# Optimization experiments

Measured on AMD Instinct MI355X. Metric: run time of the kernel, lower is better.

The kernel has to match this reference:

```python
import jax, jax.numpy as jnp
import numpy as np

D, L, C, CP, H, HD, QB, KB = 8, 2048, 128, 16, 4, 32, 32, 128
NQ = L // QB

def _ln(x, eps=1e-5):
    m = jnp.mean(x, axis=-1, keepdims=True)
    v = jnp.var(x, axis=-1, keepdims=True)
    return (x - m) * jax.lax.rsqrt(v + eps)

def _ada_ln(a, s, Wg, bg, Ws):
    # AF3 AdaLN: gated layernorm conditioned on s
    an = _ln(a); sn = _ln(s)
    return jax.nn.sigmoid(sn @ Wg + bg) * an + sn @ Ws

def setup_inputs() -> dict:
    key = jax.random.key(0)
    ks = jax.random.split(key, 32)
    p = lambda i, shape: jax.random.normal(ks[i], shape, dtype=jnp.float32) * 0.02
    inp = {}
    inp['A_I'] = jax.random.normal(ks[0], (D, L, C), dtype=jnp.float32)
    inp['S_I'] = jax.random.normal(ks[1], (D, L, C), dtype=jnp.float32)
    inp['Z_II'] = jax.random.normal(ks[2], (1, L, L, CP), dtype=jnp.float32)
    # static sliding-window indices: 128-key window centered on each 32-query block
    inp['indicesQ'] = jnp.arange(L, dtype=jnp.int64).reshape(NQ, QB)
    kraw = (jnp.arange(NQ) * QB - (KB - QB) // 2)[:, None] + jnp.arange(KB)[None, :]
    inp['indicesK'] = jnp.clip(kraw, 0, L - 1).astype(jnp.int64)
    inp['maskQ_float'] = jnp.zeros((NQ, QB), jnp.float32)
    inp['maskK_float'] = ((kraw < 0) | (kraw >= L)).astype(jnp.float32)
    # parameters
    inp['ada1_Wg'] = p(3, (C, C)); inp['ada1_bg'] = jnp.zeros((C,), jnp.float32); inp['ada1_Ws'] = p(4, (C, C))
    inp['Wq'] = p(5, (C, H * HD)); inp['bq'] = jnp.zeros((H * HD,), jnp.float32)
    inp['Wk'] = p(6, (C, H * HD)); inp['Wv'] = p(7, (C, H * HD))
    inp['ln0_g'] = jnp.ones((CP,), jnp.float32); inp['ln0_b'] = jnp.zeros((CP,), jnp.float32)
    inp['Wb'] = p(8, (CP, H))
    inp['Wg_attn'] = p(9, (C, H * HD))
    inp['Wa'] = p(10, (H * HD, C))
    inp['Wop'] = p(11, (C, C)); inp['bop'] = jnp.full((C,), -2.0, jnp.float32)
    inp['ada2_Wg'] = p(12, (C, C)); inp['ada2_bg'] = jnp.zeros((C,), jnp.float32); inp['ada2_Ws'] = p(13, (C, C))
    inp['W_sw'] = p(14, (C, 2 * C)); inp['W_lin'] = p(15, (C, 2 * C))
    inp['ct_Wg'] = p(16, (C, C)); inp['ct_bg'] = jnp.full((C,), -2.0, jnp.float32)
    inp['W_out2'] = p(17, (2 * C, C))
    return inp

def _forward(A_I, S_I, Z_II, indicesQ, indicesK, maskQ_float, maskK_float,
             ada1_Wg, ada1_bg, ada1_Ws, Wq, bq, Wk, Wv, ln0_g, ln0_b, Wb,
             Wg_attn, Wa, Wop, bop, ada2_Wg, ada2_bg, ada2_Ws, W_sw, W_lin,
             ct_Wg, ct_bg, W_out2):
    Dn, Lv = A_I.shape[0], A_I.shape[1]
    An = _ada_ln(A_I, S_I, ada1_Wg, ada1_bg, ada1_Ws)
    Q = (An @ Wq + bq).reshape(Dn, Lv, H, HD)
    K = (An @ Wk).reshape(Dn, Lv, H, HD)
    V = (An @ Wv).reshape(Dn, Lv, H, HD)
    B = ((_ln(Z_II) * ln0_g + ln0_b) @ Wb)[0]        # [L, L, H]
    G = jax.nn.sigmoid(An @ Wg_attn).reshape(Dn, Lv, H, HD)
    qs = Q[:, indicesQ]                              # [D, nq, qb, H, hd]
    ksub = K[:, indicesK]                            # [D, nq, kb, H, hd]
    vs = V[:, indicesK]
    attn = jnp.einsum('dnihc,dnjhc->dnijh', qs, ksub) / jnp.sqrt(jnp.float32(HD))
    bias = B[indicesQ[:, :, None], indicesK[:, None, :]]  # [nq, qb, kb, H]
    attn = attn + bias[None]
    mask = maskQ_float[None, :, :, None, None] + maskK_float[None, :, None, :, None]
    attn = attn - 1e9 * mask
    attn = jax.nn.softmax(attn, axis=-2)             # softmax over key window (j)
    af = jnp.einsum('dnijh,dnjhc->dnihc', attn, vs)
    af = af * (1.0 - maskQ_float)[None, :, :, None, None]
    af = af.reshape(Dn, -1, H, HD)[:, :Lv]
    af = (G * af).reshape(Dn, Lv, H * HD) @ Wa
    B_I = jax.nn.sigmoid(S_I @ Wop + bop) * af
    A = A_I + B_I
    an2 = _ada_ln(A, S_I, ada2_Wg, ada2_bg, ada2_Ws)
    b = jax.nn.silu(an2 @ W_sw) * (an2 @ W_lin)      # SwiGLU transition
    A = A + jax.nn.sigmoid(S_I @ ct_Wg + ct_bg) * (b @ W_out2)
    return A

def reference(A_I, S_I, Z_II, indicesQ, indicesK, maskQ_float, maskK_float,
              ada1_Wg, ada1_bg, ada1_Ws, Wq, bq, Wk, Wv, ln0_g, ln0_b, Wb,
              Wg_attn, Wa, Wop, bop, ada2_Wg, ada2_bg, ada2_Ws, W_sw, W_lin,
              ct_Wg, ct_bg, W_out2):
    return _forward(A_I, S_I, Z_II, indicesQ, indicesK, maskQ_float, maskK_float,
                    ada1_Wg, ada1_bg, ada1_Ws, Wq, bq, Wk, Wv, ln0_g, ln0_b, Wb,
                    Wg_attn, Wa, Wop, bop, ada2_Wg, ada2_bg, ada2_Ws, W_sw, W_lin,
                    ct_Wg, ct_bg, W_out2)
```

## Files before the change

kernel.cpp:

```cpp
#include <hip/hip_runtime.h>

#define DL 16384
#define LL 2048
#define NQB 64
#define QBS 32
#define KBS 128

typedef __attribute__((ext_vector_type(8))) short short8;
typedef __attribute__((ext_vector_type(4))) short short4v;
typedef __attribute__((ext_vector_type(4))) float f32x4;

__device__ __forceinline__ float sigmoidf_(float x) { return 1.f / (1.f + expf(-x)); }

__device__ __forceinline__ short f2bf(float f) {
    union { float f; unsigned u; } v; v.f = f;
    unsigned r = (v.u + 0x7FFFu + ((v.u >> 16) & 1u)) >> 16;
    return (short)r;
}
__device__ __forceinline__ unsigned f2bfu(float f) {
    union { float f; unsigned u; } v; v.f = f;
    return (v.u + 0x7FFFu + ((v.u >> 16) & 1u)) >> 16;
}
__device__ __forceinline__ float bf2f(short h) {
    union { unsigned u; float f; } v; v.u = ((unsigned)(unsigned short)h) << 16;
    return v.f;
}
__device__ __forceinline__ unsigned packbf16(short a, short b) {
    return ((unsigned)(unsigned short)a) | (((unsigned)(unsigned short)b) << 16);
}

#define AFRAG(buf, stride, r0, kk) (*(const short8*)&(buf)[(size_t)((r0) + cl) * (stride) + (kk) * 32 + kg * 8])
#define WFRAG(Wt, K, n0, kk) (*(const short8*)((Wt) + (size_t)((n0) + cl) * (K) + (kk) * 32 + kg * 8))
#define MFMA(acc, a, b) acc = __builtin_amdgcn_mfma_f32_16x16x32_bf16(a, b, acc, 0, 0, 0)

__global__ __launch_bounds__(256) void k_prep(
    const float* __restrict__ W0, const float* __restrict__ W1, const float* __restrict__ W2,
    const float* __restrict__ W3, const float* __restrict__ W4, const float* __restrict__ W5,
    const float* __restrict__ W6, const float* __restrict__ W7, const float* __restrict__ W8,
    const float* __restrict__ W9, const float* __restrict__ W10,
    const float* __restrict__ Wsw, const float* __restrict__ Wlin, const float* __restrict__ Wout2,
    const float* __restrict__ Z, const float* __restrict__ g16, const float* __restrict__ b16,
    const float* __restrict__ Wb,
    short* __restrict__ wout, short* __restrict__ BBt)
{
    __shared__ float sW[128 * 128];
    __shared__ float sWb[64], sg[16], sb[16];
    __shared__ short sT[4 * 4 * 128];
    const int b = blockIdx.x;
    const int tid = threadIdx.x;

    if (b < 17) {
        const float* srcs[14] = {W0,W1,W2,W3,W4,W5,W6,W7,W8,W9,W10,Wsw,Wlin,Wout2};
        const int sel[17]  = {0,1,2,3,4,5,6,7,8,9,10,11,11,12,12,13,13};
        const int soff[17] = {0,0,0,0,0,0,0,0,0,0,0, 0,128, 0,128, 0,16384};
        const int sN[17]   = {128,128,128,128,128,128,128,128,128,128,128, 256,256,256,256, 128,128};
        const int doff[17] = {0,16384,32768,49152,65536,81920,98304,114688,131072,147456,163840,
                              180224,196608, 212992,229376, 245760,245888};
        const int dK[17]   = {128,128,128,128,128,128,128,128,128,128,128, 128,128,128,128, 256,256};
        const float* src = srcs[sel[b]] + soff[b];
        const int srcN = sN[b];
        short* dst = wout + doff[b];
        const int dstK = dK[b];
        {
            const int r = tid >> 1, ch = (tid & 1) * 64;
            #pragma unroll
            for (int u = 0; u < 16; ++u) {
                float4 v = *(const float4*)(src + (size_t)r * srcN + ch + u * 4);
                *(float4*)&sW[r * 128 + ch + u * 4] = v;
            }
        }
        __syncthreads();
        {
            const int o = tid >> 1, kh = (tid & 1) * 64;
            #pragma unroll
            for (int u8 = 0; u8 < 8; ++u8) {
                short8 pk;
                #pragma unroll
                for (int e = 0; e < 8; ++e)
                    pk[e] = f2bf(sW[(kh + u8 * 8 + e) * 128 + o]);
                *(short8*)(dst + (size_t)o * dstK + kh + u8 * 8) = pk;
            }
        }
    } else {
        const int bb = b - 17;
        const int n = bb >> 3;
        const int io = (bb & 7) * 4;
        if (tid < 64) sWb[tid] = Wb[tid];
        if (tid < 16) { sg[tid] = g16[tid]; sb[tid] = b16[tid]; }
        __syncthreads();
        #pragma unroll
        for (int p = 0; p < 2; ++p) {
            int pair = tid + 256 * p;
            int il = pair >> 7, j = pair & 127;
            int i = io + il;
            int kr = n * 32 - 48 + j;
            int kc = min(max(kr, 0), LL - 1);
            const float4* z4 = (const float4*)(Z + ((long)(n * 32 + i) * LL + kc) * 16);
            float zv[16];
            #pragma unroll
            for (int w = 0; w < 4; ++w) {
                float4 v = z4[w];
                zv[w * 4 + 0] = v.x; zv[w * 4 + 1] = v.y; zv[w * 4 + 2] = v.z; zv[w * 4 + 3] = v.w;
            }
            float sm = 0.f, sq = 0.f;
            #pragma unroll
            for (int cp = 0; cp < 16; ++cp) { sm += zv[cp]; sq = fmaf(zv[cp], zv[cp], sq); }
            float m = sm * (1.f / 16.f);
            float rs = rsqrtf(sq * (1.f / 16.f) - m * m + 1e-5f);
            float b0 = 0.f, b1 = 0.f, b2 = 0.f, b3 = 0.f;
            #pragma unroll
            for (int cp = 0; cp < 16; ++cp) {
                float zn = (zv[cp] - m) * rs * sg[cp] + sb[cp];
                b0 = fmaf(zn, sWb[cp * 4 + 0], b0);
                b1 = fmaf(zn, sWb[cp * 4 + 1], b1);
                b2 = fmaf(zn, sWb[cp * 4 + 2], b2);
                b3 = fmaf(zn, sWb[cp * 4 + 3], b3);
            }
            sT[(0 * 4 + il) * 128 + j] = f2bf(b0);
            sT[(1 * 4 + il) * 128 + j] = f2bf(b1);
            sT[(2 * 4 + il) * 128 + j] = f2bf(b2);
            sT[(3 * 4 + il) * 128 + j] = f2bf(b3);
        }
        __syncthreads();
        #pragma unroll
        for (int rr = 0; rr < 2; ++rr) {
            int cid = tid + rr * 256;
            int hh = cid >> 7, j = cid & 127;
            short4v pk;
            #pragma unroll
            for (int e = 0; e < 4; ++e) pk[e] = sT[(hh * 4 + e) * 128 + j];
            *(short4v*)(BBt + (((size_t)n * 4 + hh) * 128 + j) * 32 + io) = pk;
        }
    }
}

__global__ __launch_bounds__(512) void k_adaln_qkvg(
    const float* __restrict__ A_I, const float* __restrict__ S_I,
    const short* __restrict__ Wg1t, const short* __restrict__ Ws1t,
    const short* __restrict__ Wqt, const short* __restrict__ Wkt,
    const short* __restrict__ Wvt, const short* __restrict__ Wgat,
    const float* __restrict__ bg1, const float* __restrict__ bq,
    short* __restrict__ Qo, short* __restrict__ Ko, short* __restrict__ Vo, short* __restrict__ Go)
{
    __shared__ short sAr[32 * 136];
    __shared__ short sSn[32 * 136];
    __shared__ short sAn[32 * 136];
    __shared__ float sMean[32], sRstd[32];
    const int tid = threadIdx.x;
    const int lane = tid & 63;
    const long t0 = (long)blockIdx.x * 32;

    {
        const int row = tid >> 4, seg = tid & 15;
        const float* ap = A_I + (t0 + row) * 128 + seg * 8;
        const float* sp = S_I + (t0 + row) * 128 + seg * 8;
        float av[8], sv[8];
        #pragma unroll
        for (int u = 0; u < 2; ++u) {
            float4 a4 = ((const float4*)ap)[u];
            float4 s4 = ((const float4*)sp)[u];
            av[4*u] = a4.x; av[4*u+1] = a4.y; av[4*u+2] = a4.z; av[4*u+3] = a4.w;
            sv[4*u] = s4.x; sv[4*u+1] = s4.y; sv[4*u+2] = s4.z; sv[4*u+3] = s4.w;
        }
        float am = 0.f, aq = 0.f, sm = 0.f, sq = 0.f;
        #pragma unroll
        for (int u = 0; u < 8; ++u) {
            am += av[u]; aq = fmaf(av[u], av[u], aq);
            sm += sv[u]; sq = fmaf(sv[u], sv[u], sq);
        }
        am += __shfl_xor(am, 1); am += __shfl_xor(am, 2); am += __shfl_xor(am, 4); am += __shfl_xor(am, 8);
        aq += __shfl_xor(aq, 1); aq += __shfl_xor(aq, 2); aq += __shfl_xor(aq, 4); aq += __shfl_xor(aq, 8);
        sm += __shfl_xor(sm, 1); sm += __shfl_xor(sm, 2); sm += __shfl_xor(sm, 4); sm += __shfl_xor(sm, 8);
        sq += __shfl_xor(sq, 1); sq += __shfl_xor(sq, 2); sq += __shfl_xor(sq, 4); sq += __shfl_xor(sq, 8);
        float amean = am * (1.f / 128.f);
        float arstd = rsqrtf(aq * (1.f / 128.f) - amean * amean + 1e-5f);
        float smean = sm * (1.f / 128.f);
        float srstd = rsqrtf(sq * (1.f / 128.f) - smean * smean + 1e-5f);
        if ((tid & 15) == 0) { sMean[row] = amean; sRstd[row] = arstd; }
        short8 pa, ps;
        #pragma unroll
        for (int e = 0; e < 8; ++e) {
            pa[e] = f2bf(av[e]);
            ps[e] = f2bf((sv[e] - smean) * srstd);
        }
        *(short8*)&sAr[row * 136 + seg * 8] = pa;
        *(short8*)&sSn[row * 136 + seg * 8] = ps;
    }
    __syncthreads();
    const int w = tid >> 6;
    const int n0 = w * 16;
    const int cl = lane & 15, kg = lane >> 4;
    {
        short8 wg[4], wsf[4];
        #pragma unroll
        for (int kk = 0; kk < 4; ++kk) {
            wg[kk]  = WFRAG(Wg1t, 128, n0, kk);
            wsf[kk] = WFRAG(Ws1t, 128, n0, kk);
        }
        #pragma unroll
        for (int mt = 0; mt < 2; ++mt) {
            f32x4 ag = {0.f, 0.f, 0.f, 0.f}, as = {0.f, 0.f, 0.f, 0.f};
            #pragma unroll
            for (int kk = 0; kk < 4; ++kk) {
                short8 a = AFRAG(sSn, 136, mt * 16, kk);
                MFMA(ag, a, wg[kk]);
                MFMA(as, a, wsf[kk]);
            }
            const int col = n0 + cl;
            float bgc = bg1[col];
            #pragma unroll
            for (int i = 0; i < 4; ++i) {
                int r = mt * 16 + kg * 4 + i;
                float an = (bf2f(sAr[r * 136 + col]) - sMean[r]) * sRstd[r];
                float An = sigmoidf_(ag[i] + bgc) * an + as[i];
                sAn[r * 136 + col] = f2bf(An);
            }
        }
    }
    __syncthreads();
    {
        const float SCL = 0.17677669529663687f;
        short8 af[2][4];
        #pragma unroll
        for (int mt = 0; mt < 2; ++mt)
            #pragma unroll
            for (int kk = 0; kk < 4; ++kk)
                af[mt][kk] = AFRAG(sAn, 136, mt * 16, kk);
        #pragma unroll
        for (int m = 0; m < 4; ++m) {
            const short* Wt = (m == 0) ? Wqt : (m == 1) ? Wkt : (m == 2) ? Wvt : Wgat;
            short8 wf[4];
            #pragma unroll
            for (int kk = 0; kk < 4; ++kk) wf[kk] = WFRAG(Wt, 128, n0, kk);
            #pragma unroll
            for (int mt = 0; mt < 2; ++mt) {
                f32x4 acc = {0.f, 0.f, 0.f, 0.f};
                #pragma unroll
                for (int kk = 0; kk < 4; ++kk) MFMA(acc, af[mt][kk], wf[kk]);
                const int col = n0 + cl;
                #pragma unroll
                for (int i = 0; i < 4; ++i) {
                    long t = t0 + mt * 16 + kg * 4 + i;
                    float v = acc[i];
                    if (m == 0)      Qo[t * 128 + col] = f2bf((v + bq[col]) * SCL);
                    else if (m == 1) Ko[t * 128 + col] = f2bf(v);
                    else if (m == 2) Vo[t * 128 + col] = f2bf(v);
                    else             Go[t * 128 + col] = f2bf(sigmoidf_(v));
                }
            }
        }
    }
}

__global__ __launch_bounds__(512) void k_attn_postf(
    const short* __restrict__ Qg, const short* __restrict__ Kg, const short* __restrict__ Vg,
    const short* __restrict__ Gg, const short* __restrict__ BBt, const float* __restrict__ maskK,
    const float* __restrict__ S_I, const float* __restrict__ A_I,
    const short* __restrict__ Wat, const short* __restrict__ Wopt, const short* __restrict__ ctWgt,
    const short* __restrict__ Wg2t, const short* __restrict__ Ws2t,
    const short* __restrict__ Wswt, const short* __restrict__ Wlint, const short* __restrict__ Wout2t,
    const float* __restrict__ bop, const float* __restrict__ ctbg, const float* __restrict__ bg2,
    float* __restrict__ Out)
{
    __shared__ __align__(16) char smem[78336];
    short* sAF  = (short*)smem;
    short* vts  = (short*)(smem + 8704);
    short* Pl   = (short*)(smem + 43520);
    short* sS   = (short*)(smem + 8704);
    short* sSn  = (short*)(smem + 17408);
    float* sA   = (float*)(smem + 26112);
    float* sMean = (float*)(smem + 43008);
    float* sRstd = (float*)(smem + 43136);
    short* sAn2 = sAF;
    short* sB   = (short*)(smem + 8704);

    const int n = blockIdx.x, d = blockIdx.y;
    const int tid = threadIdx.x;
    const int lane = tid & 63;
    const long tb = (long)d * LL;
    const long t0 = tb + n * 32;
    const int kbase = n * 32 - 48;
    const int cl = lane & 15, kg = lane >> 4;
    const int w = tid >> 6;
    const int h = w >> 1, amt = w & 1;

    {
        const int unit = tid >> 1, half = tid & 1;
        const int hh = unit >> 6, j0 = (unit & 63) * 2;
        int kc0 = min(max(kbase + j0, 0), LL - 1);
        int kc1 = min(max(kbase + j0 + 1, 0), LL - 1);
        const short8* p0 = (const short8*)(Vg + (tb + kc0) * 128 + hh * 32 + half * 16);
        const short8* p1 = (const short8*)(Vg + (tb + kc1) * 128 + hh * 32 + half * 16);
        short8 e0 = p0[0], e1 = p0[1];
        short8 o0 = p1[0], o1 = p1[1];
        short* vh = vts + hh * 4352;
        #pragma unroll
        for (int e = 0; e < 8; ++e)
            *(unsigned*)&vh[(half * 16 + e) * 136 + j0] = packbf16(e0[e], o0[e]);
        #pragma unroll
        for (int e = 0; e < 8; ++e)
            *(unsigned*)&vh[(half * 16 + 8 + e) * 136 + j0] = packbf16(e1[e], o1[e]);
    }

    float sc[8][4];
    {
        short8 qf = *(const short8*)(Qg + (t0 + amt * 16 + cl) * 128 + h * 32 + kg * 8);
        #pragma unroll
        for (int nt = 0; nt < 8; ++nt) {
            const int key = nt * 16 + cl;
            int kc = min(max(kbase + key, 0), LL - 1);
            short8 kf = *(const short8*)(Kg + (tb + kc) * 128 + h * 32 + kg * 8);
            float mk = maskK[n * 128 + key] * 1e9f;
            f32x4 s = {0.f, 0.f, 0.f, 0.f};
            MFMA(s, qf, kf);
            short4v bfr = *(const short4v*)(BBt + (((size_t)n * 4 + h) * 128 + key) * 32 + amt * 16 + kg * 4);
            #pragma unroll
            for (int i = 0; i < 4; ++i)
                sc[nt][i] = s[i] + bf2f(bfr[i]) - mk;
        }
    }
    {
        short* PH = Pl + h * 4352;
        #pragma unroll
        for (int i = 0; i < 4; ++i) {
            float mx = sc[0][i];
            #pragma unroll
            for (int nt = 1; nt < 8; ++nt) mx = fmaxf(mx, sc[nt][i]);
            mx = fmaxf(mx, __shfl_xor(mx, 1));
            mx = fmaxf(mx, __shfl_xor(mx, 2));
            mx = fmaxf(mx, __shfl_xor(mx, 4));
            mx = fmaxf(mx, __shfl_xor(mx, 8));
            float sm = 0.f;
            #pragma unroll
            for (int nt = 0; nt < 8; ++nt) {
                float p = __expf(sc[nt][i] - mx);
                sc[nt][i] = p; sm += p;
            }
            sm += __shfl_xor(sm, 1);
            sm += __shfl_xor(sm, 2);
            sm += __shfl_xor(sm, 4);
            sm += __shfl_xor(sm, 8);
            float inv = 1.f / sm;
            const int q = amt * 16 + kg * 4 + i;
            #pragma unroll
            for (int nt = 0; nt < 8; ++nt)
                PH[q * 136 + nt * 16 + cl] = f2bf(sc[nt][i] * inv);
        }
    }
    __syncthreads();
    {
        short* PH = Pl + h * 4352;
        short* vh = vts + h * 4352;
        #pragma unroll
        for (int ct = 0; ct < 2; ++ct) {
            f32x4 acc = {0.f, 0.f, 0.f, 0.f};
            #pragma unroll
            for (int kk = 0; kk < 4; ++kk) {
                short8 a = *(const short8*)&PH[(amt * 16 + cl) * 136 + kk * 32 + kg * 8];
                short8 b = *(const short8*)&vh[(ct * 16 + cl) * 136 + kk * 32 + kg * 8];
                MFMA(acc, a, b);
            }
            const int col = h * 32 + ct * 16 + cl;
            #pragma unroll
            for (int i = 0; i < 4; ++i) {
                int r = amt * 16 + kg * 4 + i;
                float g = bf2f(Gg[(t0 + r) * 128 + col]);
                sAF[r * 136 + col] = f2bf(g * acc[i]);
            }
        }
    }
    __syncthreads();

    {
        const int row = tid >> 4, seg = tid & 15;
        const float* apI = A_I + (t0 + row) * 128 + seg * 8;
        #pragma unroll
        for (int u = 0; u < 2; ++u)
            *(float4*)&sA[row * 132 + seg * 8 + u * 4] = ((const float4*)apI)[u];
        const float* sp = S_I + (t0 + row) * 128 + seg * 8;
        float sv[8];
        #pragma unroll
        for (int u = 0; u < 2; ++u) {
            float4 s4 = ((const float4*)sp)[u];
            sv[4*u] = s4.x; sv[4*u+1] = s4.y; sv[4*u+2] = s4.z; sv[4*u+3] = s4.w;
        }
        float sm = 0.f, sq = 0.f;
        #pragma unroll
        for (int u = 0; u < 8; ++u) { sm += sv[u]; sq = fmaf(sv[u], sv[u], sq); }
        sm += __shfl_xor(sm, 1); sm += __shfl_xor(sm, 2); sm += __shfl_xor(sm, 4); sm += __shfl_xor(sm, 8);
        sq += __shfl_xor(sq, 1); sq += __shfl_xor(sq, 2); sq += __shfl_xor(sq, 4); sq += __shfl_xor(sq, 8);
        float smean = sm * (1.f / 128.f);
        float srstd = rsqrtf(sq * (1.f / 128.f) - smean * smean + 1e-5f);
        short8 pr, pn;
        #pragma unroll
        for (int e = 0; e < 8; ++e) {
            float s = sv[e];
            pr[e] = f2bf(s);
            pn[e] = f2bf((s - smean) * srstd);
        }
        *(short8*)&sS [row * 136 + seg * 8] = pr;
        *(short8*)&sSn[row * 136 + seg * 8] = pn;
    }
    __syncthreads();
    const int n0 = w * 16;
    float g2s[8];

    {
        short8 wA[4], wO[4], wG[4];
        #pragma unroll
        for (int kk = 0; kk < 4; ++kk) {
            wA[kk] = WFRAG(Wat, 128, n0, kk);
            wO[kk] = WFRAG(Wopt, 128, n0, kk);
            wG[kk] = WFRAG(ctWgt, 128, n0, kk);
        }
        #pragma unroll
        for (int rt = 0; rt < 2; ++rt) {
            f32x4 aA = {0.f,0.f,0.f,0.f}, aO = {0.f,0.f,0.f,0.f}, aG = {0.f,0.f,0.f,0.f};
            #pragma unroll
            for (int kk = 0; kk < 4; ++kk) {
                short8 af = AFRAG(sAF, 136, rt * 16, kk);
                short8 sf = AFRAG(sS, 136, rt * 16, kk);
                MFMA(aA, af, wA[kk]);
                MFMA(aO, sf, wO[kk]);
                MFMA(aG, sf, wG[kk]);
            }
            const int col = n0 + cl;
            float bopc = bop[col], ctc = ctbg[col];
            #pragma unroll
            for (int i = 0; i < 4; ++i) {
                int r = rt * 16 + kg * 4 + i;
                float Aval = sA[r * 132 + col] + sigmoidf_(aO[i] + bopc) * aA[i];
                sA[r * 132 + col] = Aval;
                g2s[rt * 4 + i] = sigmoidf_(aG[i] + ctc);
            }
        }
    }
    __syncthreads();
    {
        const int row = tid >> 4, seg = tid & 15;
        float m = 0.f, q = 0.f;
        #pragma unroll
        for (int u = 0; u < 2; ++u) {
            float4 v = *(const float4*)&sA[row * 132 + seg * 8 + u * 4];
            m += v.x + v.y + v.z + v.w;
            q = fmaf(v.x, v.x, q); q = fmaf(v.y, v.y, q);
            q = fmaf(v.z, v.z, q); q = fmaf(v.w, v.w, q);
        }
        m += __shfl_xor(m, 1); m += __shfl_xor(m, 2); m += __shfl_xor(m, 4); m += __shfl_xor(m, 8);
        q += __shfl_xor(q, 1); q += __shfl_xor(q, 2); q += __shfl_xor(q, 4); q += __shfl_xor(q, 8);
        float mean = m * (1.f / 128.f);
        float rstd = rsqrtf(q * (1.f / 128.f) - mean * mean + 1e-5f);
        if ((tid & 15) == 0) { sMean[row] = mean; sRstd[row] = rstd; }
    }
    __syncthreads();
    {
        short8 wg2[4], ws2[4];
        #pragma unroll
        for (int kk = 0; kk < 4; ++kk) {
            wg2[kk] = WFRAG(Wg2t, 128, n0, kk);
            ws2[kk] = WFRAG(Ws2t, 128, n0, kk);
        }
        #pragma unroll
        for (int rt = 0; rt < 2; ++rt) {
            f32x4 ag = {0.f,0.f,0.f,0.f}, as = {0.f,0.f,0.f,0.f};
            #pragma unroll
            for (int kk = 0; kk < 4; ++kk) {
                short8 a = AFRAG(sSn, 136, rt * 16, kk);
                MFMA(ag, a, wg2[kk]);
                MFMA(as, a, ws2[kk]);
            }
            const int col = n0 + cl;
            float bg2c = bg2[col];
            #pragma unroll
            for (int i = 0; i < 4; ++i) {
                int r = rt * 16 + kg * 4 + i;
                float lnA = (sA[r * 132 + col] - sMean[r]) * sRstd[r];
                sAn2[r * 136 + col] = f2bf(sigmoidf_(ag[i] + bg2c) * lnA + as[i]);
            }
        }
    }
    __syncthreads();
    {
        short8 a2f[2][4];
        #pragma unroll
        for (int rt = 0; rt < 2; ++rt)
            #pragma unroll
            for (int kk = 0; kk < 4; ++kk)
                a2f[rt][kk] = AFRAG(sAn2, 136, rt * 16, kk);
        #pragma unroll
        for (int j = 0; j < 2; ++j) {
            const int n0b = w * 32 + j * 16;
            short8 ww[4], wl[4];
            #pragma unroll
            for (int kk = 0; kk < 4; ++kk) {
                ww[kk] = WFRAG(Wswt, 128, n0b, kk);
                wl[kk] = WFRAG(Wlint, 128, n0b, kk);
            }
            #pragma unroll
            for (int rt = 0; rt < 2; ++rt) {
                f32x4 aw = {0.f,0.f,0.f,0.f}, al = {0.f,0.f,0.f,0.f};
                #pragma unroll
                for (int kk = 0; kk < 4; ++kk) {
                    MFMA(aw, a2f[rt][kk], ww[kk]);
                    MFMA(al, a2f[rt][kk], wl[kk]);
                }
                const int col2 = n0b + cl;
                #pragma unroll
                for (int i = 0; i < 4; ++i) {
                    int r = rt * 16 + kg * 4 + i;
                    float x = aw[i];
                    float bb = (x / (1.f + expf(-x))) * al[i];
                    sB[r * 264 + col2] = f2bf(bb);
                }
            }
        }
    }
    __syncthreads();
    {
        short8 wo[8];
        #pragma unroll
        for (int kk = 0; kk < 8; ++kk) wo[kk] = WFRAG(Wout2t, 256, n0, kk);
        #pragma unroll
        for (int rt = 0; rt < 2; ++rt) {
            f32x4 acc = {0.f,0.f,0.f,0.f};
            #pragma unroll
            for (int kk = 0; kk < 8; ++kk) {
                short8 a = AFRAG(sB, 264, rt * 16, kk);
                MFMA(acc, a, wo[kk]);
            }
            const int col = n0 + cl;
            #pragma unroll
            for (int i = 0; i < 4; ++i) {
                int r = rt * 16 + kg * 4 + i;
                long t = t0 + r;
                Out[t * 128 + col] = sA[r * 132 + col] + g2s[rt * 4 + i] * acc[i];
            }
        }
    }
}

extern "C" void kernel_launch(void* const* d_in, const int* in_sizes, int n_in,
                              void* d_out, int out_size, void* d_ws, size_t ws_size,
                              hipStream_t stream)
{
    const float* A_I  = (const float*)d_in[0];
    const float* S_I  = (const float*)d_in[1];
    const float* Z    = (const float*)d_in[2];
    const float* maskK = (const float*)d_in[6];
    const float* a1Wg = (const float*)d_in[7];
    const float* a1bg = (const float*)d_in[8];
    const float* a1Ws = (const float*)d_in[9];
    const float* Wq   = (const float*)d_in[10];
    const float* bq   = (const float*)d_in[11];
    const float* Wk   = (const float*)d_in[12];
    const float* Wv   = (const float*)d_in[13];
    const float* ln0g = (const float*)d_in[14];
    const float* ln0b = (const float*)d_in[15];
    const float* Wb   = (const float*)d_in[16];
    const float* Wga  = (const float*)d_in[17];
    const float* Wa   = (const float*)d_in[18];
    const float* Wop  = (const float*)d_in[19];
    const float* bop  = (const float*)d_in[20];
    const float* a2Wg = (const float*)d_in[21];
    const float* a2bg = (const float*)d_in[22];
    const float* a2Ws = (const float*)d_in[23];
    const float* Wsw  = (const float*)d_in[24];
    const float* Wlin = (const float*)d_in[25];
    const float* ctWg = (const float*)d_in[26];
    const float* ctbg = (const float*)d_in[27];
    const float* Wout2 = (const float*)d_in[28];
    float* out = (float*)d_out;

    const size_t NTC = (size_t)DL * 128;
    short* Qb = (short*)d_ws;
    short* Kb = Qb + NTC;
    short* Vb = Kb + NTC;
    short* Gb = Vb + NTC;
    short* BBt = Gb + NTC;
    short* wbt = BBt + (size_t)NQB * 4 * 128 * 32;

    short* Wg1t = wbt + 0 * 16384;
    short* Ws1t = wbt + 1 * 16384;
    short* Wqt  = wbt + 2 * 16384;
    short* Wkt  = wbt + 3 * 16384;
    short* Wvt  = wbt + 4 * 16384;
    short* Wgat = wbt + 5 * 16384;
    short* Wat  = wbt + 6 * 16384;
    short* Wopt = wbt + 7 * 16384;
    short* ctWgt = wbt + 8 * 16384;
    short* Wg2t = wbt + 9 * 16384;
    short* Ws2t = wbt + 10 * 16384;
    short* Wswt = wbt + 180224;
    short* Wlint = wbt + 212992;
    short* Wout2t = wbt + 245760;

    k_prep<<<529, 256, 0, stream>>>(a1Wg, a1Ws, Wq, Wk, Wv, Wga, Wa, Wop, ctWg,
                                    a2Wg, a2Ws, Wsw, Wlin, Wout2,
                                    Z, ln0g, ln0b, Wb, wbt, BBt);
    k_adaln_qkvg<<<DL / 32, 512, 0, stream>>>(A_I, S_I, Wg1t, Ws1t, Wqt, Wkt, Wvt, Wgat,
                                              a1bg, bq, Qb, Kb, Vb, Gb);
    k_attn_postf<<<dim3(NQB, 8), 512, 0, stream>>>(Qb, Kb, Vb, Gb, BBt, maskK,
                                                   S_I, A_I,
                                                   Wat, Wopt, ctWgt, Wg2t, Ws2t,
                                                   Wswt, Wlint, Wout2t,
                                                   bop, ctbg, a2bg, out);
}
```

Measured before the change: 70.35 us.

## Swap MFMA operands to transpose accumulators and vectorize epilogue stores

Every MFMA now takes the weight fragment as the A operand and the activation as the B operand. Each lane therefore holds four consecutive output columns for one token instead of four tokens for one column. All epilogues become 4-wide vector loads and stores of bias, mask, gate and output, and the softmax row reductions now shuffle across lane groups 16 and 32. The pair-bias buffer layout is transposed to match. This reduces scattered scalar global and LDS traffic, at the cost of re-deriving index mappings across several stages, which carries a correctness risk.

```diff
diff --git a/kernel.cpp b/kernel.cpp
--- a/kernel.cpp
+++ b/kernel.cpp
@@ -16,10 +16,6 @@
     union { float f; unsigned u; } v; v.f = f;
     unsigned r = (v.u + 0x7FFFu + ((v.u >> 16) & 1u)) >> 16;
     return (short)r;
-}
-__device__ __forceinline__ unsigned f2bfu(float f) {
-    union { float f; unsigned u; } v; v.f = f;
-    return (v.u + 0x7FFFu + ((v.u >> 16) & 1u)) >> 16;
 }
 __device__ __forceinline__ float bf2f(short h) {
     union { unsigned u; float f; } v; v.u = ((unsigned)(unsigned short)h) << 16;
@@ -125,11 +121,10 @@
         #pragma unroll
         for (int rr = 0; rr < 2; ++rr) {
             int cid = tid + rr * 256;
-            int hh = cid >> 7, j = cid & 127;
-            short4v pk;
-            #pragma unroll
-            for (int e = 0; e < 4; ++e) pk[e] = sT[(hh * 4 + e) * 128 + j];
-            *(short4v*)(BBt + (((size_t)n * 4 + hh) * 128 + j) * 32 + io) = pk;
+            int hh = cid >> 7, rem = cid & 127;
+            int il = rem >> 5, jb = (rem & 31) * 4;
+            short4v pk = *(const short4v*)&sT[(hh * 4 + il) * 128 + jb];
+            *(short4v*)(BBt + (((size_t)n * 4 + hh) * 32 + io + il) * 128 + jb) = pk;
         }
     }
 }
@@ -203,18 +198,22 @@
             #pragma unroll
             for (int kk = 0; kk < 4; ++kk) {
                 short8 a = AFRAG(sSn, 136, mt * 16, kk);
-                MFMA(ag, a, wg[kk]);
-                MFMA(as, a, wsf[kk]);
-            }
-            const int col = n0 + cl;
-            float bgc = bg1[col];
+                MFMA(ag, wg[kk], a);
+                MFMA(as, wsf[kk], a);
+            }
+            const int tok = mt * 16 + cl;
+            const int c0 = n0 + kg * 4;
+            float4 bg4 = *(const float4*)&bg1[c0];
+            float mean = sMean[tok], rstd = sRstd[tok];
+            short4v ar4 = *(const short4v*)&sAr[tok * 136 + c0];
+            short4v o;
             #pragma unroll
             for (int i = 0; i < 4; ++i) {
-                int r = mt * 16 + kg * 4 + i;
-                float an = (bf2f(sAr[r * 136 + col]) - sMean[r]) * sRstd[r];
-                float An = sigmoidf_(ag[i] + bgc) * an + as[i];
-                sAn[r * 136 + col] = f2bf(An);
-            }
+                float an = (bf2f(ar4[i]) - mean) * rstd;
+                float An = sigmoidf_(ag[i] + ((const float*)&bg4)[i]) * an + as[i];
+                o[i] = f2bf(An);
+            }
+            *(short4v*)&sAn[tok * 136 + c0] = o;
         }
     }
     __syncthreads();
@@ -226,6 +225,8 @@
             #pragma unroll
             for (int kk = 0; kk < 4; ++kk)
                 af[mt][kk] = AFRAG(sAn, 136, mt * 16, kk);
+        const int c0 = n0 + kg * 4;
+        float4 bq4 = *(const float4*)&bq[c0];
         #pragma unroll
         for (int m = 0; m < 4; ++m) {
             const short* Wt = (m == 0) ? Wqt : (m == 1) ? Wkt : (m == 2) ? Wvt : Wgat;
@@ -236,16 +237,25 @@
             for (int mt = 0; mt < 2; ++mt) {
                 f32x4 acc = {0.f, 0.f, 0.f, 0.f};
                 #pragma unroll
-                for (int kk = 0; kk < 4; ++kk) MFMA(acc, af[mt][kk], wf[kk]);
-                const int col = n0 + cl;
-                #pragma unroll
-                for (int i = 0; i < 4; ++i) {
-                    long t = t0 + mt * 16 + kg * 4 + i;
-                    float v = acc[i];
-                    if (m == 0)      Qo[t * 128 + col] = f2bf((v + bq[col]) * SCL);
-                    else if (m == 1) Ko[t * 128 + col] = f2bf(v);
-                    else if (m == 2) Vo[t * 128 + col] = f2bf(v);
-                    else             Go[t * 128 + col] = f2bf(sigmoidf_(v));
+                for (int kk = 0; kk < 4; ++kk) MFMA(acc, wf[kk], af[mt][kk]);
+                long t = t0 + mt * 16 + cl;
+                short4v o;
+                if (m == 0) {
+                    #pragma unroll
+                    for (int i = 0; i < 4; ++i) o[i] = f2bf((acc[i] + ((const float*)&bq4)[i]) * SCL);
+                    *(short4v*)(Qo + t * 128 + c0) = o;
+                } else if (m == 1) {
+                    #pragma unroll
+                    for (int i = 0; i < 4; ++i) o[i] = f2bf(acc[i]);
+                    *(short4v*)(Ko + t * 128 + c0) = o;
+                } else if (m == 2) {
+                    #pragma unroll
+                    for (int i = 0; i < 4; ++i) o[i] = f2bf(acc[i]);
+                    *(short4v*)(Vo + t * 128 + c0) = o;
+                } else {
+                    #pragma unroll
+                    for (int i = 0; i < 4; ++i) o[i] = f2bf(sigmoidf_(acc[i]));
+                    *(short4v*)(Go + t * 128 + c0) = o;
                 }
             }
         }
@@ -307,66 +317,69 @@
         short8 qf = *(const short8*)(Qg + (t0 + amt * 16 + cl) * 128 + h * 32 + kg * 8);
         #pragma unroll
         for (int nt = 0; nt < 8; ++nt) {
-            const int key = nt * 16 + cl;
-            int kc = min(max(kbase + key, 0), LL - 1);
+            int kc = min(max(kbase + nt * 16 + cl, 0), LL - 1);
             short8 kf = *(const short8*)(Kg + (tb + kc) * 128 + h * 32 + kg * 8);
-            float mk = maskK[n * 128 + key] * 1e9f;
             f32x4 s = {0.f, 0.f, 0.f, 0.f};
-            MFMA(s, qf, kf);
-            short4v bfr = *(const short4v*)(BBt + (((size_t)n * 4 + h) * 128 + key) * 32 + amt * 16 + kg * 4);
+            MFMA(s, kf, qf);
+            float4 mk4 = *(const float4*)(maskK + n * 128 + nt * 16 + kg * 4);
+            short4v bfr = *(const short4v*)(BBt + (((size_t)n * 4 + h) * 32 + amt * 16 + cl) * 128 + nt * 16 + kg * 4);
             #pragma unroll
             for (int i = 0; i < 4; ++i)
-                sc[nt][i] = s[i] + bf2f(bfr[i]) - mk;
-        }
-    }
-    {
-        short* PH = Pl + h * 4352;
-        #pragma unroll
-        for (int i = 0; i < 4; ++i) {
-            float mx = sc[0][i];
-            #pragma unroll
-            for (int nt = 1; nt < 8; ++nt) mx = fmaxf(mx, sc[nt][i]);
-            mx = fmaxf(mx, __shfl_xor(mx, 1));
-            mx = fmaxf(mx, __shfl_xor(mx, 2));
-            mx = fmaxf(mx, __shfl_xor(mx, 4));
-            mx = fmaxf(mx, __shfl_xor(mx, 8));
-            float sm = 0.f;
-            #pragma unroll
-            for (int nt = 0; nt < 8; ++nt) {
+                sc[nt][i] = s[i] + bf2f(bfr[i]) - ((const float*)&mk4)[i] * 1e9f;
+        }
+    }
+    {
+        float mx = sc[0][0];
+        #pragma unroll
+        for (int nt = 0; nt < 8; ++nt)
+            #pragma unroll
+            for (int i = 0; i < 4; ++i) mx = fmaxf(mx, sc[nt][i]);
+        mx = fmaxf(mx, __shfl_xor(mx, 16));
+        mx = fmaxf(mx, __shfl_xor(mx, 32));
+        float sm = 0.f;
+        #pragma unroll
+        for (int nt = 0; nt < 8; ++nt)
+            #pragma unroll
+            for (int i = 0; i < 4; ++i) {
                 float p = __expf(sc[nt][i] - mx);
                 sc[nt][i] = p; sm += p;
             }
-            sm += __shfl_xor(sm, 1);
-            sm += __shfl_xor(sm, 2);
-            sm += __shfl_xor(sm, 4);
-            sm += __shfl_xor(sm, 8);
-            float inv = 1.f / sm;
-            const int q = amt * 16 + kg * 4 + i;
-            #pragma unroll
-            for (int nt = 0; nt < 8; ++nt)
-                PH[q * 136 + nt * 16 + cl] = f2bf(sc[nt][i] * inv);
+        sm += __shfl_xor(sm, 16);
+        sm += __shfl_xor(sm, 32);
+        float inv = 1.f / sm;
+        short* PH = Pl + h * 4352;
+        const int tok = amt * 16 + cl;
+        #pragma unroll
+        for (int nt = 0; nt < 8; ++nt) {
+            short4v p4;
+            #pragma unroll
+            for (int i = 0; i < 4; ++i) p4[i] = f2bf(sc[nt][i] * inv);
+            *(short4v*)&PH[tok * 136 + nt * 16 + kg * 4] = p4;
         }
     }
     __syncthreads();
     {
         short* PH = Pl + h * 4352;
         short* vh = vts + h * 4352;
+        const int tok = amt * 16 + cl;
+        short8 pfr[4];
+        #pragma unroll
+        for (int kk = 0; kk < 4; ++kk)
+            pfr[kk] = *(const short8*)&PH[tok * 136 + kk * 32 + kg * 8];
         #pragma unroll
         for (int ct = 0; ct < 2; ++ct) {
             f32x4 acc = {0.f, 0.f, 0.f, 0.f};
             #pragma unroll
             for (int kk = 0; kk < 4; ++kk) {
-                short8 a = *(const short8*)&PH[(amt * 16 + cl) * 136 + kk * 32 + kg * 8];
-                short8 b = *(const short8*)&vh[(ct * 16 + cl) * 136 + kk * 32 + kg * 8];
-                MFMA(acc, a, b);
-            }
-            const int col = h * 32 + ct * 16 + cl;
-            #pragma unroll
-            for (int i = 0; i < 4; ++i) {
-                int r = amt * 16 + kg * 4 + i;
-                float g = bf2f(Gg[(t0 + r) * 128 + col]);
-                sAF[r * 136 + col] = f2bf(g * acc[i]);
-            }
+                short8 a = *(const short8*)&vh[(ct * 16 + cl) * 136 + kk * 32 + kg * 8];
+                MFMA(acc, a, pfr[kk]);
+            }
+            const int c0 = h * 32 + ct * 16 + kg * 4;
+            short4v g4 = *(const short4v*)(Gg + (t0 + tok) * 128 + c0);
+            short4v o4;
+            #pragma unroll
+            for (int i = 0; i < 4; ++i) o4[i] = f2bf(bf2f(g4[i]) * acc[i]);
+            *(short4v*)&sAF[tok * 136 + c0] = o4;
         }
     }
     __syncthreads();
@@ -403,6 +416,7 @@
     }
     __syncthreads();
     const int n0 = w * 16;
+    const int c0 = n0 + kg * 4;
     float g2s[8];
 
     {
@@ -413,6 +427,8 @@
             wO[kk] = WFRAG(Wopt, 128, n0, kk);
             wG[kk] = WFRAG(ctWgt, 128, n0, kk);
         }
+        float4 bop4 = *(const float4*)&bop[c0];
+        float4 ct4  = *(const float4*)&ctbg[c0];
         #pragma unroll
         for (int rt = 0; rt < 2; ++rt) {
             f32x4 aA = {0.f,0.f,0.f,0.f}, aO = {0.f,0.f,0.f,0.f}, aG = {0.f,0.f,0.f,0.f};
@@ -420,19 +436,20 @@
             for (int kk = 0; kk < 4; ++kk) {
                 short8 af = AFRAG(sAF, 136, rt * 16, kk);
                 short8 sf = AFRAG(sS, 136, rt * 16, kk);
-                MFMA(aA, af, wA[kk]);
-                MFMA(aO, sf, wO[kk]);
-                MFMA(aG, sf, wG[kk]);
-            }
-            const int col = n0 + cl;
-            float bopc = bop[col], ctc = ctbg[col];
+                MFMA(aA, wA[kk], af);
+                MFMA(aO, wO[kk], sf);
+                MFMA(aG, wG[kk], sf);
+            }
+            const int tok = rt * 16 + cl;
+            float4 Av = *(const float4*)&sA[tok * 132 + c0];
+            float4 outv;
             #pragma unroll
             for (int i = 0; i < 4; ++i) {
-                int r = rt * 16 + kg * 4 + i;
-                float Aval = sA[r * 132 + col] + sigmoidf_(aO[i] + bopc) * aA[i];
-                sA[r * 132 + col] = Aval;
-                g2s[rt * 4 + i] = sigmoidf_(aG[i] + ctc);
-            }
+                ((float*)&outv)[i] = ((const float*)&Av)[i]
+                    + sigmoidf_(aO[i] + ((const float*)&bop4)[i]) * aA[i];
+                g2s[rt * 4 + i] = sigmoidf_(aG[i] + ((const float*)&ct4)[i]);
+            }
+            *(float4*)&sA[tok * 132 + c0] = outv;
         }
     }
     __syncthreads();
@@ -460,23 +477,26 @@
             wg2[kk] = WFRAG(Wg2t, 128, n0, kk);
             ws2[kk] = WFRAG(Ws2t, 128, n0, kk);
         }
+        float4 bg24 = *(const float4*)&bg2[c0];
         #pragma unroll
         for (int rt = 0; rt < 2; ++rt) {
             f32x4 ag = {0.f,0.f,0.f,0.f}, as = {0.f,0.f,0.f,0.f};
             #pragma unroll
             for (int kk = 0; kk < 4; ++kk) {
                 short8 a = AFRAG(sSn, 136, rt * 16, kk);
-                MFMA(ag, a, wg2[kk]);
-                MFMA(as, a, ws2[kk]);
-            }
-            const int col = n0 + cl;
-            float bg2c = bg2[col];
+                MFMA(ag, wg2[kk], a);
+                MFMA(as, ws2[kk], a);
+            }
+            const int tok = rt * 16 + cl;
+            float mean = sMean[tok], rstd = sRstd[tok];
+            float4 Av = *(const float4*)&sA[tok * 132 + c0];
+            short4v o;
             #pragma unroll
             for (int i = 0; i < 4; ++i) {
-                int r = rt * 16 + kg * 4 + i;
-                float lnA = (sA[r * 132 + col] - sMean[r]) * sRstd[r];
-                sAn2[r * 136 + col] = f2bf(sigmoidf_(ag[i] + bg2c) * lnA + as[i]);
-            }
+                float lnA = (((const float*)&Av)[i] - mean) * rstd;
+                o[i] = f2bf(sigmoidf_(ag[i] + ((const float*)&bg24)[i]) * lnA + as[i]);
+            }
+            *(short4v*)&sAn2[tok * 136 + c0] = o;
         }
     }
     __syncthreads();
@@ -501,17 +521,17 @@
                 f32x4 aw = {0.f,0.f,0.f,0.f}, al = {0.f,0.f,0.f,0.f};
                 #pragma unroll
                 for (int kk = 0; kk < 4; ++kk) {
-                    MFMA(aw, a2f[rt][kk], ww[kk]);
-                    MFMA(al, a2f[rt][kk], wl[kk]);
+                    MFMA(aw, ww[kk], a2f[rt][kk]);
+                    MFMA(al, wl[kk], a2f[rt][kk]);
                 }
-                const int col2 = n0b + cl;
+                const int tok = rt * 16 + cl;
+                short4v o;
                 #pragma unroll
                 for (int i = 0; i < 4; ++i) {
-                    int r = rt * 16 + kg * 4 + i;
                     float x = aw[i];
-                    float bb = (x / (1.f + expf(-x))) * al[i];
-                    sB[r * 264 + col2] = f2bf(bb);
+                    o[i] = f2bf((x / (1.f + expf(-x))) * al[i]);
                 }
+                *(short4v*)&sB[tok * 264 + n0b + kg * 4] = o;
             }
         }
     }
@@ -526,15 +546,15 @@
             #pragma unroll
             for (int kk = 0; kk < 8; ++kk) {
                 short8 a = AFRAG(sB, 264, rt * 16, kk);
-                MFMA(acc, a, wo[kk]);
-            }
-            const int col = n0 + cl;
-            #pragma unroll
-            for (int i = 0; i < 4; ++i) {
-                int r = rt * 16 + kg * 4 + i;
-                long t = t0 + r;
-                Out[t * 128 + col] = sA[r * 132 + col] + g2s[rt * 4 + i] * acc[i];
-            }
+                MFMA(acc, wo[kk], a);
+            }
+            const int tok = rt * 16 + cl;
+            float4 Av = *(const float4*)&sA[tok * 132 + c0];
+            float4 outv;
+            #pragma unroll
+            for (int i = 0; i < 4; ++i)
+                ((float*)&outv)[i] = ((const float*)&Av)[i] + g2s[rt * 4 + i] * acc[i];
+            *(float4*)(Out + (t0 + tok) * 128 + c0) = outv;
         }
     }
 }
@@ -577,7 +597,7 @@
     short* Vb = Kb + NTC;
     short* Gb = Vb + NTC;
     short* BBt = Gb + NTC;
-    short* wbt = BBt + (size_t)NQB * 4 * 128 * 32;
+    short* wbt = BBt + (size_t)NQB * 4 * 32 * 128;
 
     short* Wg1t = wbt + 0 * 16384;
     short* Ws1t = wbt + 1 * 16384;
```

Result: no change. 71.22 us (+1.2%).
